# Optimization experiments

Measured on AMD Instinct MI355X. Metric: run time of the kernel, lower is better.

Reference implementation:

```python
import jax, jax.numpy as jnp
import numpy as np

TEMPERATURE = 8.0  # sqrt(head_dim=64)
NEG_INF = -1000000000.0


def setup_inputs() -> dict:
    key = jax.random.key(0)
    kq, kk, kv, km = jax.random.split(key, 4)
    B, H, S, D = 2, 16, 2048, 64
    q = jax.random.normal(kq, (B, H, S, D), dtype=jnp.float32)
    k = jax.random.normal(kk, (B, H, S, D), dtype=jnp.float32)
    v = jax.random.normal(kv, (B, H, S, D), dtype=jnp.float32)
    mask = jax.random.randint(km, (B, 1, S, S), 0, 2, dtype=jnp.int32)
    return {"q": q, "k": k, "v": v, "mask": mask}


def reference(q, k, v, mask):
    # scores: [B,H,S,S] = (q/T) @ k^T
    attn = jnp.einsum('bhqd,bhkd->bhqk', q / TEMPERATURE, k)
    attn = jnp.where(mask == 0, NEG_INF, attn)
    attn = jax.nn.softmax(attn, axis=-1)  # dropout is identity in eval mode
    output = jnp.einsum('bhqk,bhkd->bhqd', attn, v)
    return (output, attn)
```

## Files before the change

kernel.cpp:

```cpp
#include <hip/hip_runtime.h>
#include <hip/hip_bf16.h>


using short4v = __attribute__((ext_vector_type(4))) short;
using short8v = __attribute__((ext_vector_type(8))) short;
using float4v = __attribute__((ext_vector_type(4))) float;

#define S_LEN 2048
#define D_DIM 64
#define QT 64
#define KTILE 64
#define NIT (S_LEN / KTILE)
#define NW (S_LEN / 64)
#define LDK 72
#define ATTN_OFF (2 * 16 * 2048 * 64)
#define TILE_SH (KTILE * D_DIM)

typedef __attribute__((address_space(1))) const unsigned int gu32;
typedef __attribute__((address_space(3))) unsigned int lu32;

__device__ __forceinline__ short f2bf(float x) {
  __hip_bfloat16 h = __float2bfloat16(x);
  return __builtin_bit_cast(short, h);
}
__device__ __forceinline__ float bf2f(short s) {
  return __builtin_bit_cast(float, ((unsigned)(unsigned short)s) << 16);
}

__global__ __launch_bounds__(256) void pack_mask_kernel(
    const int* __restrict__ mask, unsigned long long* __restrict__ pm, int nwords) {
  const int lane = threadIdx.x & 63;
  int gw = (blockIdx.x * blockDim.x + threadIdx.x) >> 6;
  const int stride = (gridDim.x * blockDim.x) >> 6;
  for (int w = gw; w < nwords; w += stride) {
    int m = mask[(size_t)w * 64 + lane];
    unsigned long long bits = __ballot(m != 0);
    if (lane == 0) pm[w] = bits;
  }
}

__global__ __launch_bounds__(256) void kprep_kernel(
    const float* __restrict__ k, short* __restrict__ kbs) {
  int g = blockIdx.x * 256 + threadIdx.x;
  int kr = g >> 3;
  int slot = g & 7;
  const float* src = k + (size_t)kr * D_DIM + ((slot ^ (kr & 7)) << 3);
  float4v a = *(const float4v*)src;
  float4v b = *(const float4v*)(src + 4);
  short8v t;
  t[0] = f2bf(a[0]); t[1] = f2bf(a[1]); t[2] = f2bf(a[2]); t[3] = f2bf(a[3]);
  t[4] = f2bf(b[0]); t[5] = f2bf(b[1]); t[6] = f2bf(b[2]); t[7] = f2bf(b[3]);
  *(short8v*)(kbs + (size_t)g * 8) = t;
}

__global__ __launch_bounds__(256) void vprep_kernel(
    const float* __restrict__ v, short* __restrict__ vts) {
  __shared__ short lds_t[64 * 72];
  const int tid = threadIdx.x;
  const int bh = blockIdx.x >> 5;
  const int kt = blockIdx.x & 31;
  const float* vp = v + ((size_t)bh * S_LEN + kt * KTILE) * D_DIM;
#pragma unroll
  for (int i = 0; i < 4; ++i) {
    int idx = tid + i * 256;
    int s = idx >> 4;
    int d0 = (idx & 15) * 4;
    float4v x = *(const float4v*)(vp + (size_t)s * D_DIM + d0);
#pragma unroll
    for (int j = 0; j < 4; ++j) lds_t[(d0 + j) * 72 + s] = f2bf(x[j]);
  }
  __syncthreads();
  short* dst = vts + (size_t)blockIdx.x * TILE_SH;
#pragma unroll
  for (int i = 0; i < 2; ++i) {
    int g = tid + i * 256;
    int d = g >> 3;
    int slot = g & 7;
    int lsrc = slot ^ (d & 7);
    short8v t = *(const short8v*)(lds_t + d * 72 + lsrc * 8);
    *(short8v*)(dst + g * 8) = t;
  }
}

__device__ __forceinline__ void stage_wave(const short* __restrict__ g, short* l,
                                           int wave, int lane) {
  const short* s0 = g + wave * 1024 + lane * 8;
  short* d0 = l + wave * 1024;
  __builtin_amdgcn_global_load_lds((gu32*)s0, (lu32*)d0, 16, 0, 0);
  __builtin_amdgcn_global_load_lds((gu32*)(s0 + 512), (lu32*)(d0 + 512), 16, 0, 0);
}

__global__ __launch_bounds__(256, 3) void sdpa_fused(
    const float* __restrict__ q, const short* __restrict__ kbs,
    const short* __restrict__ vts, const unsigned long long* __restrict__ pm,
    float* __restrict__ out) {
  __shared__ __align__(16) short lds_k[2][TILE_SH];
  __shared__ __align__(16) short lds_vt[2][TILE_SH];
  __shared__ short lds_p[QT * LDK];

  const int tid  = threadIdx.x;
  const int wave = tid >> 6;
  const int lane = tid & 63;
  const int quad = lane >> 4;
  const int l16  = lane & 15;

  const int blk = (blockIdx.x & 7) * 128 + (blockIdx.x >> 3);
  const int qt  = blk & (NIT - 1);
  const int bh  = blk >> 5;
  const int b   = bh >> 4;

  const float* qp = q + (size_t)bh * S_LEN * D_DIM;
  const short* kb_g = kbs + (size_t)bh * S_LEN * D_DIM;
  const short* vt_g = vts + (size_t)bh * (NIT * TILE_SH);
  float* outO = out + (size_t)bh * S_LEN * D_DIM;
  float* outA = out + (size_t)ATTN_OFF + (size_t)bh * S_LEN * S_LEN;

  const int qbase = qt * QT;
  const int qrowC = qbase + wave * 16 + quad * 4;

  const float QSCALE = 0.18033688011112042f;
  short8v qa[2];
  {
    const int qrow = qbase + wave * 16 + l16;
    const float* src = qp + (size_t)qrow * D_DIM + quad * 8;
#pragma unroll
    for (int c = 0; c < 2; ++c) {
      float4v x0 = *(const float4v*)(src + c * 32);
      float4v x1 = *(const float4v*)(src + c * 32 + 4);
      short8v t;
      t[0] = f2bf(x0[0] * QSCALE); t[1] = f2bf(x0[1] * QSCALE);
      t[2] = f2bf(x0[2] * QSCALE); t[3] = f2bf(x0[3] * QSCALE);
      t[4] = f2bf(x1[0] * QSCALE); t[5] = f2bf(x1[1] * QSCALE);
      t[6] = f2bf(x1[2] * QSCALE); t[7] = f2bf(x1[3] * QSCALE);
      qa[c] = t;
    }
  }

  const unsigned long long* pmrow = pm + ((size_t)b * S_LEN + qrowC) * NW;

  float lsum[4] = {0.f, 0.f, 0.f, 0.f};
  unsigned long long mrow_c[4], mrow_n[4];
#pragma unroll
  for (int r = 0; r < 4; ++r) mrow_c[r] = pmrow[(size_t)r * NW];
  stage_wave(kb_g, lds_k[0], wave, lane);
  __syncthreads();

#pragma unroll 1
  for (int kt = 0; kt < NIT; ++kt) {
    if (kt + 1 < NIT) {
#pragma unroll
      for (int r = 0; r < 4; ++r) mrow_n[r] = pmrow[(size_t)r * NW + kt + 1];
      stage_wave(kb_g + (kt + 1) * TILE_SH, lds_k[(kt + 1) & 1], wave, lane);
    }
    const short* kbuf = lds_k[kt & 1];
#pragma unroll
    for (int t = 0; t < 4; ++t) {
      float4v acc = {0.f, 0.f, 0.f, 0.f};
      const int row = t * 16 + l16;
      const int sw = (row & 7) << 3;
#pragma unroll
      for (int c = 0; c < 2; ++c) {
        short8v bf = *(const short8v*)(kbuf + row * 64 + (((c * 32) + quad * 8) ^ sw));
        acc = __builtin_amdgcn_mfma_f32_16x16x32_bf16(qa[c], bf, acc, 0, 0, 0);
      }
#pragma unroll
      for (int r = 0; r < 4; ++r) {
        bool mv = ((mrow_c[r] >> (t * 16 + l16)) & 1ull) != 0;
        float p = mv ? exp2f(acc[r]) : 0.f;
        lsum[r] += p;
      }
    }
#pragma unroll
    for (int r = 0; r < 4; ++r) mrow_c[r] = mrow_n[r];
    __syncthreads();
  }

  float invl[4];
#pragma unroll
  for (int r = 0; r < 4; ++r) {
    float s = lsum[r];
    s += __shfl_xor(s, 1);
    s += __shfl_xor(s, 2);
    s += __shfl_xor(s, 4);
    s += __shfl_xor(s, 8);
    invl[r] = 1.0f / s;
  }

  float4v oacc[4];
#pragma unroll
  for (int dt = 0; dt < 4; ++dt) oacc[dt] = (float4v){0.f, 0.f, 0.f, 0.f};

#pragma unroll
  for (int r = 0; r < 4; ++r) mrow_c[r] = pmrow[(size_t)r * NW];
  stage_wave(kb_g, lds_k[0], wave, lane);
  stage_wave(vt_g, lds_vt[0], wave, lane);
  __syncthreads();

#pragma unroll 1
  for (int kt = 0; kt < NIT; ++kt) {
    if (kt + 1 < NIT) {
#pragma unroll
      for (int r = 0; r < 4; ++r) mrow_n[r] = pmrow[(size_t)r * NW + kt + 1];
      stage_wave(kb_g + (kt + 1) * TILE_SH, lds_k[(kt + 1) & 1], wave, lane);
      stage_wave(vt_g + (kt + 1) * TILE_SH, lds_vt[(kt + 1) & 1], wave, lane);
    }
    const short* kbuf = lds_k[kt & 1];
    const short* vbuf = lds_vt[kt & 1];

#pragma unroll
    for (int t = 0; t < 4; ++t) {
      float4v acc = {0.f, 0.f, 0.f, 0.f};
      const int row = t * 16 + l16;
      const int sw = (row & 7) << 3;
#pragma unroll
      for (int c = 0; c < 2; ++c) {
        short8v bf = *(const short8v*)(kbuf + row * 64 + (((c * 32) + quad * 8) ^ sw));
        acc = __builtin_amdgcn_mfma_f32_16x16x32_bf16(qa[c], bf, acc, 0, 0, 0);
      }
      short* prow = lds_p + (wave * 16 + quad * 4) * LDK + t * 16 + l16;
#pragma unroll
      for (int r = 0; r < 4; ++r) {
        bool mv = ((mrow_c[r] >> (t * 16 + l16)) & 1ull) != 0;
        float p = mv ? exp2f(acc[r]) * invl[r] : 0.f;
        prow[r * LDK] = f2bf(p);
      }
    }

    {
      const int row16 = lane >> 2;
      const int cg = (lane & 3) * 16;
      const short* src = lds_p + (wave * 16 + row16) * LDK + cg;
      short8v p0 = *(const short8v*)src;
      short8v p1 = *(const short8v*)(src + 8);
      float* arow = outA + (size_t)(qbase + wave * 16 + row16) * S_LEN + kt * KTILE + cg;
      float4v f0 = {bf2f(p0[0]), bf2f(p0[1]), bf2f(p0[2]), bf2f(p0[3])};
      float4v f1 = {bf2f(p0[4]), bf2f(p0[5]), bf2f(p0[6]), bf2f(p0[7])};
      float4v f2 = {bf2f(p1[0]), bf2f(p1[1]), bf2f(p1[2]), bf2f(p1[3])};
      float4v f3 = {bf2f(p1[4]), bf2f(p1[5]), bf2f(p1[6]), bf2f(p1[7])};
      *(float4v*)(arow)      = f0;
      *(float4v*)(arow + 4)  = f1;
      *(float4v*)(arow + 8)  = f2;
      *(float4v*)(arow + 12) = f3;
    }

#pragma unroll
    for (int c = 0; c < 2; ++c) {
      short8v pa = *(const short8v*)(lds_p + (wave * 16 + l16) * LDK + c * 32 + quad * 8);
#pragma unroll
      for (int dt = 0; dt < 4; ++dt) {
        const int row = dt * 16 + l16;
        const int sw = (row & 7) << 3;
        short8v vb = *(const short8v*)(vbuf + row * 64 + (((c * 32) + quad * 8) ^ sw));
        oacc[dt] = __builtin_amdgcn_mfma_f32_16x16x32_bf16(pa, vb, oacc[dt], 0, 0, 0);
      }
    }
#pragma unroll
    for (int r = 0; r < 4; ++r) mrow_c[r] = mrow_n[r];
    __syncthreads();
  }

  {
    float* orow = outO + (size_t)qrowC * D_DIM + l16;
#pragma unroll
    for (int dt = 0; dt < 4; ++dt) {
#pragma unroll
      for (int r = 0; r < 4; ++r) {
        orow[(size_t)r * D_DIM + dt * 16] = oacc[dt][r];
      }
    }
  }
}

template <bool PACKED>
__global__ __launch_bounds__(256, 4) void sdpa_kernel(
    const float* __restrict__ q, const float* __restrict__ k,
    const float* __restrict__ v, const int* __restrict__ mask,
    const unsigned long long* __restrict__ pm, float* __restrict__ out) {
  __shared__ short lds_k[KTILE * LDK];
  __shared__ short lds_vt[D_DIM * LDK];
  __shared__ short lds_p[QT * LDK];

  const int tid  = threadIdx.x;
  const int wave = tid >> 6;
  const int lane = tid & 63;
  const int quad = lane >> 4;
  const int l16  = lane & 15;

  const int blk = blockIdx.x;
  const int qt  = blk & (NIT - 1);
  const int bh  = blk >> 5;
  const int b   = bh >> 4;

  const float* qp = q + (size_t)bh * S_LEN * D_DIM;
  const float* kp = k + (size_t)bh * S_LEN * D_DIM;
  const float* vp = v + (size_t)bh * S_LEN * D_DIM;
  const int*   mp = mask + (size_t)b * S_LEN * S_LEN;
  float* outO = out + (size_t)bh * S_LEN * D_DIM;
  float* outA = out + (size_t)ATTN_OFF + (size_t)bh * S_LEN * S_LEN;

  const int qbase = qt * QT;
  const int qrowC = qbase + wave * 16 + quad * 4;

  const float QSCALE = 0.18033688011112042f;
  short8v qa[2];
  {
    const int qrow = qbase + wave * 16 + l16;
    const float* src = qp + (size_t)qrow * D_DIM + quad * 8;
#pragma unroll
    for (int c = 0; c < 2; ++c) {
      float4v x0 = *(const float4v*)(src + c * 32);
      float4v x1 = *(const float4v*)(src + c * 32 + 4);
      short8v t;
      t[0] = f2bf(x0[0] * QSCALE); t[1] = f2bf(x0[1] * QSCALE);
      t[2] = f2bf(x0[2] * QSCALE); t[3] = f2bf(x0[3] * QSCALE);
      t[4] = f2bf(x1[0] * QSCALE); t[5] = f2bf(x1[1] * QSCALE);
      t[6] = f2bf(x1[2] * QSCALE); t[7] = f2bf(x1[3] * QSCALE);
      qa[c] = t;
    }
  }

  float lsum[4] = {0.f, 0.f, 0.f, 0.f};

#pragma unroll 1
  for (int kt = 0; kt < NIT; ++kt) {
#pragma unroll
    for (int i = 0; i < 4; ++i) {
      int f = tid + i * 256;
      int row = f >> 4;
      int col = (f & 15) * 4;
      float4v x = *(const float4v*)(kp + (size_t)(kt * KTILE + row) * D_DIM + col);
      short4v y;
      y[0] = f2bf(x[0]); y[1] = f2bf(x[1]); y[2] = f2bf(x[2]); y[3] = f2bf(x[3]);
      *(short4v*)(lds_k + row * LDK + col) = y;
    }
    __syncthreads();

    unsigned long long mrow[4];
    if (PACKED) {
#pragma unroll
      for (int r = 0; r < 4; ++r)
        mrow[r] = pm[((size_t)b * S_LEN + qrowC + r) * NW + kt];
    }
#pragma unroll
    for (int t = 0; t < 4; ++t) {
      float4v acc = {0.f, 0.f, 0.f, 0.f};
#pragma unroll
      for (int c = 0; c < 2; ++c) {
        short8v bf = *(const short8v*)(lds_k + (t * 16 + l16) * LDK + c * 32 + quad * 8);
        acc = __builtin_amdgcn_mfma_f32_16x16x32_bf16(qa[c], bf, acc, 0, 0, 0);
      }
      const int kcol = kt * KTILE + t * 16 + l16;
#pragma unroll
      for (int r = 0; r < 4; ++r) {
        bool mv = PACKED ? (((mrow[r] >> (t * 16 + l16)) & 1ull) != 0)
                         : (mp[(size_t)(qrowC + r) * S_LEN + kcol] != 0);
        float p = mv ? exp2f(acc[r]) : 0.f;
        lsum[r] += p;
      }
    }
    __syncthreads();
  }

  float invl[4];
#pragma unroll
  for (int r = 0; r < 4; ++r) {
    float s = lsum[r];
    s += __shfl_xor(s, 1);
    s += __shfl_xor(s, 2);
    s += __shfl_xor(s, 4);
    s += __shfl_xor(s, 8);
    invl[r] = 1.0f / s;
  }

  float4v oacc[4];
#pragma unroll
  for (int dt = 0; dt < 4; ++dt) oacc[dt] = (float4v){0.f, 0.f, 0.f, 0.f};

#pragma unroll 1
  for (int kt = 0; kt < NIT; ++kt) {
#pragma unroll
    for (int i = 0; i < 4; ++i) {
      int f = tid + i * 256;
      int row = f >> 4;
      int col = (f & 15) * 4;
      float4v x = *(const float4v*)(kp + (size_t)(kt * KTILE + row) * D_DIM + col);
      short4v y;
      y[0] = f2bf(x[0]); y[1] = f2bf(x[1]); y[2] = f2bf(x[2]); y[3] = f2bf(x[3]);
      *(short4v*)(lds_k + row * LDK + col) = y;
    }
    {
      const int d = tid & 63;
      const int krg = (tid >> 6) * 4;
#pragma unroll
      for (int i = 0; i < 4; ++i) {
        int kr0 = i * 16 + krg;
        short4v y;
#pragma unroll
        for (int j = 0; j < 4; ++j) {
          float x = vp[(size_t)(kt * KTILE + kr0 + j) * D_DIM + d];
          y[j] = f2bf(x);
        }
        *(short4v*)(lds_vt + d * LDK + kr0) = y;
      }
    }
    __syncthreads();

    unsigned long long mrow[4];
    if (PACKED) {
#pragma unroll
      for (int r = 0; r < 4; ++r)
        mrow[r] = pm[((size_t)b * S_LEN + qrowC + r) * NW + kt];
    }
#pragma unroll
    for (int t = 0; t < 4; ++t) {
      float4v acc = {0.f, 0.f, 0.f, 0.f};
#pragma unroll
      for (int c = 0; c < 2; ++c) {
        short8v bf = *(const short8v*)(lds_k + (t * 16 + l16) * LDK + c * 32 + quad * 8);
        acc = __builtin_amdgcn_mfma_f32_16x16x32_bf16(qa[c], bf, acc, 0, 0, 0);
      }
      const int kcol = kt * KTILE + t * 16 + l16;
      short* prow = lds_p + (wave * 16 + quad * 4) * LDK + t * 16 + l16;
#pragma unroll
      for (int r = 0; r < 4; ++r) {
        bool mv = PACKED ? (((mrow[r] >> (t * 16 + l16)) & 1ull) != 0)
                         : (mp[(size_t)(qrowC + r) * S_LEN + kcol] != 0);
        float p = mv ? exp2f(acc[r]) * invl[r] : 0.f;
        prow[r * LDK] = f2bf(p);
      }
    }

    {
      const int row16 = lane >> 2;
      const int cg = (lane & 3) * 16;
      const short* src = lds_p + (wave * 16 + row16) * LDK + cg;
      short8v p0 = *(const short8v*)src;
      short8v p1 = *(const short8v*)(src + 8);
      float* arow = outA + (size_t)(qbase + wave * 16 + row16) * S_LEN + kt * KTILE + cg;
      float4v f0 = {bf2f(p0[0]), bf2f(p0[1]), bf2f(p0[2]), bf2f(p0[3])};
      float4v f1 = {bf2f(p0[4]), bf2f(p0[5]), bf2f(p0[6]), bf2f(p0[7])};
      float4v f2 = {bf2f(p1[0]), bf2f(p1[1]), bf2f(p1[2]), bf2f(p1[3])};
      float4v f3 = {bf2f(p1[4]), bf2f(p1[5]), bf2f(p1[6]), bf2f(p1[7])};
      *(float4v*)(arow)      = f0;
      *(float4v*)(arow + 4)  = f1;
      *(float4v*)(arow + 8)  = f2;
      *(float4v*)(arow + 12) = f3;
    }

#pragma unroll
    for (int c = 0; c < 2; ++c) {
      short8v pa = *(const short8v*)(lds_p + (wave * 16 + l16) * LDK + c * 32 + quad * 8);
#pragma unroll
      for (int dt = 0; dt < 4; ++dt) {
        short8v vb = *(const short8v*)(lds_vt + (dt * 16 + l16) * LDK + c * 32 + quad * 8);
        oacc[dt] = __builtin_amdgcn_mfma_f32_16x16x32_bf16(pa, vb, oacc[dt], 0, 0, 0);
      }
    }
    __syncthreads();
  }

  {
    float* orow = outO + (size_t)qrowC * D_DIM + l16;
#pragma unroll
    for (int dt = 0; dt < 4; ++dt) {
#pragma unroll
      for (int r = 0; r < 4; ++r) {
        orow[(size_t)r * D_DIM + dt * 16] = oacc[dt][r];
      }
    }
  }
}

extern "C" void kernel_launch(void* const* d_in, const int* in_sizes, int n_in,
                              void* d_out, int out_size, void* d_ws, size_t ws_size,
                              hipStream_t stream) {
  const float* q = (const float*)d_in[0];
  const float* k = (const float*)d_in[1];
  const float* v = (const float*)d_in[2];
  const int* mask = (const int*)d_in[3];
  float* out = (float*)d_out;

  const int BH = 2 * 16;
  dim3 grid(BH * (S_LEN / QT));
  dim3 block(256);

  const int nwords = 2 * S_LEN * NW;
  const size_t pm_bytes = (size_t)nwords * 8;
  const size_t kbs_bytes = (size_t)BH * S_LEN * D_DIM * 2;
  const size_t kbs_off = pm_bytes;
  const size_t vts_off = kbs_off + kbs_bytes;
  const size_t need = vts_off + kbs_bytes;

  if (ws_size >= need) {
    unsigned long long* pm = (unsigned long long*)d_ws;
    short* kbs = (short*)((char*)d_ws + kbs_off);
    short* vts = (short*)((char*)d_ws + vts_off);
    pack_mask_kernel<<<256, 256, 0, stream>>>(mask, pm, nwords);
    kprep_kernel<<<2048, 256, 0, stream>>>(k, kbs);
    vprep_kernel<<<1024, 256, 0, stream>>>(v, vts);
    sdpa_fused<<<grid, block, 0, stream>>>(q, kbs, vts, pm, out);
  } else if (ws_size >= pm_bytes) {
    unsigned long long* pm = (unsigned long long*)d_ws;
    pack_mask_kernel<<<256, 256, 0, stream>>>(mask, pm, nwords);
    sdpa_kernel<true><<<grid, block, 0, stream>>>(q, k, v, mask, pm, out);
  } else {
    sdpa_kernel<false><<<grid, block, 0, stream>>>(q, k, v, mask, nullptr, out);
  }
}
```

Before: 845.5 us.

## Merge prep kernels into one launch and defer nontemporal attention stores

Combines the mask packing, K conversion and V transpose kernels into a single launch that dispatches on block index, removing two kernel launches and their gaps. In the fused SDPA kernel, the fp32 attention-probability stores for each tile are moved to the start of the next iteration so the writes overlap with the next tile's loads and MFMA work. The attention and output writes also become nontemporal stores to avoid polluting the cache. The deferred stores keep extra registers live across iterations, which may affect occupancy.

```diff
diff --git a/kernel.cpp b/kernel.cpp
--- a/kernel.cpp
+++ b/kernel.cpp
@@ -27,6 +27,61 @@
   return __builtin_bit_cast(float, ((unsigned)(unsigned short)s) << 16);
 }
 
+__global__ __launch_bounds__(256) void prep_kernel(
+    const float* __restrict__ k, const float* __restrict__ v,
+    const int* __restrict__ mask, short* __restrict__ kbs,
+    short* __restrict__ vts, unsigned long long* __restrict__ pm, int nwords) {
+  __shared__ short lds_t[64 * 72];
+  const int tid = threadIdx.x;
+  const int bid = blockIdx.x;
+  if (bid < 2048) {
+    int g = bid * 256 + tid;
+    int kr = g >> 3;
+    int slot = g & 7;
+    const float* src = k + (size_t)kr * D_DIM + ((slot ^ (kr & 7)) << 3);
+    float4v a = *(const float4v*)src;
+    float4v b = *(const float4v*)(src + 4);
+    short8v t;
+    t[0] = f2bf(a[0]); t[1] = f2bf(a[1]); t[2] = f2bf(a[2]); t[3] = f2bf(a[3]);
+    t[4] = f2bf(b[0]); t[5] = f2bf(b[1]); t[6] = f2bf(b[2]); t[7] = f2bf(b[3]);
+    *(short8v*)(kbs + (size_t)g * 8) = t;
+  } else if (bid < 3072) {
+    const int vb = bid - 2048;
+    const int bh = vb >> 5;
+    const int kt = vb & 31;
+    const float* vp = v + ((size_t)bh * S_LEN + kt * KTILE) * D_DIM;
+#pragma unroll
+    for (int i = 0; i < 4; ++i) {
+      int idx = tid + i * 256;
+      int s = idx >> 4;
+      int d0 = (idx & 15) * 4;
+      float4v x = *(const float4v*)(vp + (size_t)s * D_DIM + d0);
+#pragma unroll
+      for (int j = 0; j < 4; ++j) lds_t[(d0 + j) * 72 + s] = f2bf(x[j]);
+    }
+    __syncthreads();
+    short* dst = vts + (size_t)vb * TILE_SH;
+#pragma unroll
+    for (int i = 0; i < 2; ++i) {
+      int g = tid + i * 256;
+      int d = g >> 3;
+      int slot = g & 7;
+      int lsrc = slot ^ (d & 7);
+      short8v t = *(const short8v*)(lds_t + d * 72 + lsrc * 8);
+      *(short8v*)(dst + g * 8) = t;
+    }
+  } else {
+    const int lane = tid & 63;
+    int gw = ((bid - 3072) * 256 + tid) >> 6;
+    const int stride = (256 * 256) >> 6;
+    for (int w = gw; w < nwords; w += stride) {
+      int m = mask[(size_t)w * 64 + lane];
+      unsigned long long bits = __ballot(m != 0);
+      if (lane == 0) pm[w] = bits;
+    }
+  }
+}
+
 __global__ __launch_bounds__(256) void pack_mask_kernel(
     const int* __restrict__ mask, unsigned long long* __restrict__ pm, int nwords) {
   const int lane = threadIdx.x & 63;
@@ -39,49 +94,6 @@
   }
 }
 
-__global__ __launch_bounds__(256) void kprep_kernel(
-    const float* __restrict__ k, short* __restrict__ kbs) {
-  int g = blockIdx.x * 256 + threadIdx.x;
-  int kr = g >> 3;
-  int slot = g & 7;
-  const float* src = k + (size_t)kr * D_DIM + ((slot ^ (kr & 7)) << 3);
-  float4v a = *(const float4v*)src;
-  float4v b = *(const float4v*)(src + 4);
-  short8v t;
-  t[0] = f2bf(a[0]); t[1] = f2bf(a[1]); t[2] = f2bf(a[2]); t[3] = f2bf(a[3]);
-  t[4] = f2bf(b[0]); t[5] = f2bf(b[1]); t[6] = f2bf(b[2]); t[7] = f2bf(b[3]);
-  *(short8v*)(kbs + (size_t)g * 8) = t;
-}
-
-__global__ __launch_bounds__(256) void vprep_kernel(
-    const float* __restrict__ v, short* __restrict__ vts) {
-  __shared__ short lds_t[64 * 72];
-  const int tid = threadIdx.x;
-  const int bh = blockIdx.x >> 5;
-  const int kt = blockIdx.x & 31;
-  const float* vp = v + ((size_t)bh * S_LEN + kt * KTILE) * D_DIM;
-#pragma unroll
-  for (int i = 0; i < 4; ++i) {
-    int idx = tid + i * 256;
-    int s = idx >> 4;
-    int d0 = (idx & 15) * 4;
-    float4v x = *(const float4v*)(vp + (size_t)s * D_DIM + d0);
-#pragma unroll
-    for (int j = 0; j < 4; ++j) lds_t[(d0 + j) * 72 + s] = f2bf(x[j]);
-  }
-  __syncthreads();
-  short* dst = vts + (size_t)blockIdx.x * TILE_SH;
-#pragma unroll
-  for (int i = 0; i < 2; ++i) {
-    int g = tid + i * 256;
-    int d = g >> 3;
-    int slot = g & 7;
-    int lsrc = slot ^ (d & 7);
-    short8v t = *(const short8v*)(lds_t + d * 72 + lsrc * 8);
-    *(short8v*)(dst + g * 8) = t;
-  }
-}
-
 __device__ __forceinline__ void stage_wave(const short* __restrict__ g, short* l,
                                            int wave, int lane) {
   const short* s0 = g + wave * 1024 + lane * 8;
@@ -139,7 +151,8 @@
   const unsigned long long* pmrow = pm + ((size_t)b * S_LEN + qrowC) * NW;
 
   float lsum[4] = {0.f, 0.f, 0.f, 0.f};
-  unsigned long long mrow_c[4], mrow_n[4];
+  unsigned long long mrow_c[4];
+  unsigned long long mrow_n[4] = {0ull, 0ull, 0ull, 0ull};
 #pragma unroll
   for (int r = 0; r < 4; ++r) mrow_c[r] = pmrow[(size_t)r * NW];
   stage_wave(kb_g, lds_k[0], wave, lane);
@@ -196,8 +209,24 @@
   stage_wave(vt_g, lds_vt[0], wave, lane);
   __syncthreads();
 
+  const int row16 = lane >> 2;
+  const int cg = (lane & 3) * 16;
+  float* arow_base = outA + (size_t)(qbase + wave * 16 + row16) * S_LEN + cg;
+  short8v pp0, pp1;
+
 #pragma unroll 1
   for (int kt = 0; kt < NIT; ++kt) {
+    if (kt > 0) {
+      float* arow = arow_base + (kt - 1) * KTILE;
+      float4v f0 = {bf2f(pp0[0]), bf2f(pp0[1]), bf2f(pp0[2]), bf2f(pp0[3])};
+      float4v f1 = {bf2f(pp0[4]), bf2f(pp0[5]), bf2f(pp0[6]), bf2f(pp0[7])};
+      float4v f2 = {bf2f(pp1[0]), bf2f(pp1[1]), bf2f(pp1[2]), bf2f(pp1[3])};
+      float4v f3 = {bf2f(pp1[4]), bf2f(pp1[5]), bf2f(pp1[6]), bf2f(pp1[7])};
+      __builtin_nontemporal_store(f0, (float4v*)(arow));
+      __builtin_nontemporal_store(f1, (float4v*)(arow + 4));
+      __builtin_nontemporal_store(f2, (float4v*)(arow + 8));
+      __builtin_nontemporal_store(f3, (float4v*)(arow + 12));
+    }
     if (kt + 1 < NIT) {
 #pragma unroll
       for (int r = 0; r < 4; ++r) mrow_n[r] = pmrow[(size_t)r * NW + kt + 1];
@@ -221,6 +250,211 @@
 #pragma unroll
       for (int r = 0; r < 4; ++r) {
         bool mv = ((mrow_c[r] >> (t * 16 + l16)) & 1ull) != 0;
+        float p = mv ? exp2f(acc[r]) * invl[r] : 0.f;
+        prow[r * LDK] = f2bf(p);
+      }
+    }
+
+    {
+      const short* src = lds_p + (wave * 16 + row16) * LDK + cg;
+      pp0 = *(const short8v*)src;
+      pp1 = *(const short8v*)(src + 8);
+    }
+
+#pragma unroll
+    for (int c = 0; c < 2; ++c) {
+      short8v pa = *(const short8v*)(lds_p + (wave * 16 + l16) * LDK + c * 32 + quad * 8);
+#pragma unroll
+      for (int dt = 0; dt < 4; ++dt) {
+        const int row = dt * 16 + l16;
+        const int sw = (row & 7) << 3;
+        short8v vb = *(const short8v*)(vbuf + row * 64 + (((c * 32) + quad * 8) ^ sw));
+        oacc[dt] = __builtin_amdgcn_mfma_f32_16x16x32_bf16(pa, vb, oacc[dt], 0, 0, 0);
+      }
+    }
+#pragma unroll
+    for (int r = 0; r < 4; ++r) mrow_c[r] = mrow_n[r];
+    __syncthreads();
+  }
+
+  {
+    float* arow = arow_base + (NIT - 1) * KTILE;
+    float4v f0 = {bf2f(pp0[0]), bf2f(pp0[1]), bf2f(pp0[2]), bf2f(pp0[3])};
+    float4v f1 = {bf2f(pp0[4]), bf2f(pp0[5]), bf2f(pp0[6]), bf2f(pp0[7])};
+    float4v f2 = {bf2f(pp1[0]), bf2f(pp1[1]), bf2f(pp1[2]), bf2f(pp1[3])};
+    float4v f3 = {bf2f(pp1[4]), bf2f(pp1[5]), bf2f(pp1[6]), bf2f(pp1[7])};
+    __builtin_nontemporal_store(f0, (float4v*)(arow));
+    __builtin_nontemporal_store(f1, (float4v*)(arow + 4));
+    __builtin_nontemporal_store(f2, (float4v*)(arow + 8));
+    __builtin_nontemporal_store(f3, (float4v*)(arow + 12));
+  }
+
+  {
+    float* orow = outO + (size_t)qrowC * D_DIM + l16;
+#pragma unroll
+    for (int dt = 0; dt < 4; ++dt) {
+#pragma unroll
+      for (int r = 0; r < 4; ++r) {
+        __builtin_nontemporal_store(oacc[dt][r], orow + (size_t)r * D_DIM + dt * 16);
+      }
+    }
+  }
+}
+
+template <bool PACKED>
+__global__ __launch_bounds__(256, 4) void sdpa_kernel(
+    const float* __restrict__ q, const float* __restrict__ k,
+    const float* __restrict__ v, const int* __restrict__ mask,
+    const unsigned long long* __restrict__ pm, float* __restrict__ out) {
+  __shared__ short lds_k[KTILE * LDK];
+  __shared__ short lds_vt[D_DIM * LDK];
+  __shared__ short lds_p[QT * LDK];
+
+  const int tid  = threadIdx.x;
+  const int wave = tid >> 6;
+  const int lane = tid & 63;
+  const int quad = lane >> 4;
+  const int l16  = lane & 15;
+
+  const int blk = blockIdx.x;
+  const int qt  = blk & (NIT - 1);
+  const int bh  = blk >> 5;
+  const int b   = bh >> 4;
+
+  const float* qp = q + (size_t)bh * S_LEN * D_DIM;
+  const float* kp = k + (size_t)bh * S_LEN * D_DIM;
+  const float* vp = v + (size_t)bh * S_LEN * D_DIM;
+  const int*   mp = mask + (size_t)b * S_LEN * S_LEN;
+  float* outO = out + (size_t)bh * S_LEN * D_DIM;
+  float* outA = out + (size_t)ATTN_OFF + (size_t)bh * S_LEN * S_LEN;
+
+  const int qbase = qt * QT;
+  const int qrowC = qbase + wave * 16 + quad * 4;
+
+  const float QSCALE = 0.18033688011112042f;
+  short8v qa[2];
+  {
+    const int qrow = qbase + wave * 16 + l16;
+    const float* src = qp + (size_t)qrow * D_DIM + quad * 8;
+#pragma unroll
+    for (int c = 0; c < 2; ++c) {
+      float4v x0 = *(const float4v*)(src + c * 32);
+      float4v x1 = *(const float4v*)(src + c * 32 + 4);
+      short8v t;
+      t[0] = f2bf(x0[0] * QSCALE); t[1] = f2bf(x0[1] * QSCALE);
+      t[2] = f2bf(x0[2] * QSCALE); t[3] = f2bf(x0[3] * QSCALE);
+      t[4] = f2bf(x1[0] * QSCALE); t[5] = f2bf(x1[1] * QSCALE);
+      t[6] = f2bf(x1[2] * QSCALE); t[7] = f2bf(x1[3] * QSCALE);
+      qa[c] = t;
+    }
+  }
+
+  float lsum[4] = {0.f, 0.f, 0.f, 0.f};
+
+#pragma unroll 1
+  for (int kt = 0; kt < NIT; ++kt) {
+#pragma unroll
+    for (int i = 0; i < 4; ++i) {
+      int f = tid + i * 256;
+      int row = f >> 4;
+      int col = (f & 15) * 4;
+      float4v x = *(const float4v*)(kp + (size_t)(kt * KTILE + row) * D_DIM + col);
+      short4v y;
+      y[0] = f2bf(x[0]); y[1] = f2bf(x[1]); y[2] = f2bf(x[2]); y[3] = f2bf(x[3]);
+      *(short4v*)(lds_k + row * LDK + col) = y;
+    }
+    __syncthreads();
+
+    unsigned long long mrow[4];
+    if (PACKED) {
+#pragma unroll
+      for (int r = 0; r < 4; ++r)
+        mrow[r] = pm[((size_t)b * S_LEN + qrowC + r) * NW + kt];
+    }
+#pragma unroll
+    for (int t = 0; t < 4; ++t) {
+      float4v acc = {0.f, 0.f, 0.f, 0.f};
+#pragma unroll
+      for (int c = 0; c < 2; ++c) {
+        short8v bf = *(const short8v*)(lds_k + (t * 16 + l16) * LDK + c * 32 + quad * 8);
+        acc = __builtin_amdgcn_mfma_f32_16x16x32_bf16(qa[c], bf, acc, 0, 0, 0);
+      }
+      const int kcol = kt * KTILE + t * 16 + l16;
+#pragma unroll
+      for (int r = 0; r < 4; ++r) {
+        bool mv = PACKED ? (((mrow[r] >> (t * 16 + l16)) & 1ull) != 0)
+                         : (mp[(size_t)(qrowC + r) * S_LEN + kcol] != 0);
+        float p = mv ? exp2f(acc[r]) : 0.f;
+        lsum[r] += p;
+      }
+    }
+    __syncthreads();
+  }
+
+  float invl[4];
+#pragma unroll
+  for (int r = 0; r < 4; ++r) {
+    float s = lsum[r];
+    s += __shfl_xor(s, 1);
+    s += __shfl_xor(s, 2);
+    s += __shfl_xor(s, 4);
+    s += __shfl_xor(s, 8);
+    invl[r] = 1.0f / s;
+  }
+
+  float4v oacc[4];
+#pragma unroll
+  for (int dt = 0; dt < 4; ++dt) oacc[dt] = (float4v){0.f, 0.f, 0.f, 0.f};
+
+#pragma unroll 1
+  for (int kt = 0; kt < NIT; ++kt) {
+#pragma unroll
+    for (int i = 0; i < 4; ++i) {
+      int f = tid + i * 256;
+      int row = f >> 4;
+      int col = (f & 15) * 4;
+      float4v x = *(const float4v*)(kp + (size_t)(kt * KTILE + row) * D_DIM + col);
+      short4v y;
+      y[0] = f2bf(x[0]); y[1] = f2bf(x[1]); y[2] = f2bf(x[2]); y[3] = f2bf(x[3]);
+      *(short4v*)(lds_k + row * LDK + col) = y;
+    }
+    {
+      const int d = tid & 63;
+      const int krg = (tid >> 6) * 4;
+#pragma unroll
+      for (int i = 0; i < 4; ++i) {
+        int kr0 = i * 16 + krg;
+        short4v y;
+#pragma unroll
+        for (int j = 0; j < 4; ++j) {
+          float x = vp[(size_t)(kt * KTILE + kr0 + j) * D_DIM + d];
+          y[j] = f2bf(x);
+        }
+        *(short4v*)(lds_vt + d * LDK + kr0) = y;
+      }
+    }
+    __syncthreads();
+
+    unsigned long long mrow[4];
+    if (PACKED) {
+#pragma unroll
+      for (int r = 0; r < 4; ++r)
+        mrow[r] = pm[((size_t)b * S_LEN + qrowC + r) * NW + kt];
+    }
+#pragma unroll
+    for (int t = 0; t < 4; ++t) {
+      float4v acc = {0.f, 0.f, 0.f, 0.f};
+#pragma unroll
+      for (int c = 0; c < 2; ++c) {
+        short8v bf = *(const short8v*)(lds_k + (t * 16 + l16) * LDK + c * 32 + quad * 8);
+        acc = __builtin_amdgcn_mfma_f32_16x16x32_bf16(qa[c], bf, acc, 0, 0, 0);
+      }
+      const int kcol = kt * KTILE + t * 16 + l16;
+      short* prow = lds_p + (wave * 16 + quad * 4) * LDK + t * 16 + l16;
+#pragma unroll
+      for (int r = 0; r < 4; ++r) {
+        bool mv = PACKED ? (((mrow[r] >> (t * 16 + l16)) & 1ull) != 0)
+                         : (mp[(size_t)(qrowC + r) * S_LEN + kcol] != 0);
         float p = mv ? exp2f(acc[r]) * invl[r] : 0.f;
         prow[r * LDK] = f2bf(p);
       }
@@ -248,210 +482,6 @@
       short8v pa = *(const short8v*)(lds_p + (wave * 16 + l16) * LDK + c * 32 + quad * 8);
 #pragma unroll
       for (int dt = 0; dt < 4; ++dt) {
-        const int row = dt * 16 + l16;
-        const int sw = (row & 7) << 3;
-        short8v vb = *(const short8v*)(vbuf + row * 64 + (((c * 32) + quad * 8) ^ sw));
-        oacc[dt] = __builtin_amdgcn_mfma_f32_16x16x32_bf16(pa, vb, oacc[dt], 0, 0, 0);
-      }
-    }
-#pragma unroll
-    for (int r = 0; r < 4; ++r) mrow_c[r] = mrow_n[r];
-    __syncthreads();
-  }
-
-  {
-    float* orow = outO + (size_t)qrowC * D_DIM + l16;
-#pragma unroll
-    for (int dt = 0; dt < 4; ++dt) {
-#pragma unroll
-      for (int r = 0; r < 4; ++r) {
-        orow[(size_t)r * D_DIM + dt * 16] = oacc[dt][r];
-      }
-    }
-  }
-}
-
-template <bool PACKED>
-__global__ __launch_bounds__(256, 4) void sdpa_kernel(
-    const float* __restrict__ q, const float* __restrict__ k,
-    const float* __restrict__ v, const int* __restrict__ mask,
-    const unsigned long long* __restrict__ pm, float* __restrict__ out) {
-  __shared__ short lds_k[KTILE * LDK];
-  __shared__ short lds_vt[D_DIM * LDK];
-  __shared__ short lds_p[QT * LDK];
-
-  const int tid  = threadIdx.x;
-  const int wave = tid >> 6;
-  const int lane = tid & 63;
-  const int quad = lane >> 4;
-  const int l16  = lane & 15;
-
-  const int blk = blockIdx.x;
-  const int qt  = blk & (NIT - 1);
-  const int bh  = blk >> 5;
-  const int b   = bh >> 4;
-
-  const float* qp = q + (size_t)bh * S_LEN * D_DIM;
-  const float* kp = k + (size_t)bh * S_LEN * D_DIM;
-  const float* vp = v + (size_t)bh * S_LEN * D_DIM;
-  const int*   mp = mask + (size_t)b * S_LEN * S_LEN;
-  float* outO = out + (size_t)bh * S_LEN * D_DIM;
-  float* outA = out + (size_t)ATTN_OFF + (size_t)bh * S_LEN * S_LEN;
-
-  const int qbase = qt * QT;
-  const int qrowC = qbase + wave * 16 + quad * 4;
-
-  const float QSCALE = 0.18033688011112042f;
-  short8v qa[2];
-  {
-    const int qrow = qbase + wave * 16 + l16;
-    const float* src = qp + (size_t)qrow * D_DIM + quad * 8;
-#pragma unroll
-    for (int c = 0; c < 2; ++c) {
-      float4v x0 = *(const float4v*)(src + c * 32);
-      float4v x1 = *(const float4v*)(src + c * 32 + 4);
-      short8v t;
-      t[0] = f2bf(x0[0] * QSCALE); t[1] = f2bf(x0[1] * QSCALE);
-      t[2] = f2bf(x0[2] * QSCALE); t[3] = f2bf(x0[3] * QSCALE);
-      t[4] = f2bf(x1[0] * QSCALE); t[5] = f2bf(x1[1] * QSCALE);
-      t[6] = f2bf(x1[2] * QSCALE); t[7] = f2bf(x1[3] * QSCALE);
-      qa[c] = t;
-    }
-  }
-
-  float lsum[4] = {0.f, 0.f, 0.f, 0.f};
-
-#pragma unroll 1
-  for (int kt = 0; kt < NIT; ++kt) {
-#pragma unroll
-    for (int i = 0; i < 4; ++i) {
-      int f = tid + i * 256;
-      int row = f >> 4;
-      int col = (f & 15) * 4;
-      float4v x = *(const float4v*)(kp + (size_t)(kt * KTILE + row) * D_DIM + col);
-      short4v y;
-      y[0] = f2bf(x[0]); y[1] = f2bf(x[1]); y[2] = f2bf(x[2]); y[3] = f2bf(x[3]);
-      *(short4v*)(lds_k + row * LDK + col) = y;
-    }
-    __syncthreads();
-
-    unsigned long long mrow[4];
-    if (PACKED) {
-#pragma unroll
-      for (int r = 0; r < 4; ++r)
-        mrow[r] = pm[((size_t)b * S_LEN + qrowC + r) * NW + kt];
-    }
-#pragma unroll
-    for (int t = 0; t < 4; ++t) {
-      float4v acc = {0.f, 0.f, 0.f, 0.f};
-#pragma unroll
-      for (int c = 0; c < 2; ++c) {
-        short8v bf = *(const short8v*)(lds_k + (t * 16 + l16) * LDK + c * 32 + quad * 8);
-        acc = __builtin_amdgcn_mfma_f32_16x16x32_bf16(qa[c], bf, acc, 0, 0, 0);
-      }
-      const int kcol = kt * KTILE + t * 16 + l16;
-#pragma unroll
-      for (int r = 0; r < 4; ++r) {
-        bool mv = PACKED ? (((mrow[r] >> (t * 16 + l16)) & 1ull) != 0)
-                         : (mp[(size_t)(qrowC + r) * S_LEN + kcol] != 0);
-        float p = mv ? exp2f(acc[r]) : 0.f;
-        lsum[r] += p;
-      }
-    }
-    __syncthreads();
-  }
-
-  float invl[4];
-#pragma unroll
-  for (int r = 0; r < 4; ++r) {
-    float s = lsum[r];
-    s += __shfl_xor(s, 1);
-    s += __shfl_xor(s, 2);
-    s += __shfl_xor(s, 4);
-    s += __shfl_xor(s, 8);
-    invl[r] = 1.0f / s;
-  }
-
-  float4v oacc[4];
-#pragma unroll
-  for (int dt = 0; dt < 4; ++dt) oacc[dt] = (float4v){0.f, 0.f, 0.f, 0.f};
-
-#pragma unroll 1
-  for (int kt = 0; kt < NIT; ++kt) {
-#pragma unroll
-    for (int i = 0; i < 4; ++i) {
-      int f = tid + i * 256;
-      int row = f >> 4;
-      int col = (f & 15) * 4;
-      float4v x = *(const float4v*)(kp + (size_t)(kt * KTILE + row) * D_DIM + col);
-      short4v y;
-      y[0] = f2bf(x[0]); y[1] = f2bf(x[1]); y[2] = f2bf(x[2]); y[3] = f2bf(x[3]);
-      *(short4v*)(lds_k + row * LDK + col) = y;
-    }
-    {
-      const int d = tid & 63;
-      const int krg = (tid >> 6) * 4;
-#pragma unroll
-      for (int i = 0; i < 4; ++i) {
-        int kr0 = i * 16 + krg;
-        short4v y;
-#pragma unroll
-        for (int j = 0; j < 4; ++j) {
-          float x = vp[(size_t)(kt * KTILE + kr0 + j) * D_DIM + d];
-          y[j] = f2bf(x);
-        }
-        *(short4v*)(lds_vt + d * LDK + kr0) = y;
-      }
-    }
-    __syncthreads();
-
-    unsigned long long mrow[4];
-    if (PACKED) {
-#pragma unroll
-      for (int r = 0; r < 4; ++r)
-        mrow[r] = pm[((size_t)b * S_LEN + qrowC + r) * NW + kt];
-    }
-#pragma unroll
-    for (int t = 0; t < 4; ++t) {
-      float4v acc = {0.f, 0.f, 0.f, 0.f};
-#pragma unroll
-      for (int c = 0; c < 2; ++c) {
-        short8v bf = *(const short8v*)(lds_k + (t * 16 + l16) * LDK + c * 32 + quad * 8);
-        acc = __builtin_amdgcn_mfma_f32_16x16x32_bf16(qa[c], bf, acc, 0, 0, 0);
-      }
-      const int kcol = kt * KTILE + t * 16 + l16;
-      short* prow = lds_p + (wave * 16 + quad * 4) * LDK + t * 16 + l16;
-#pragma unroll
-      for (int r = 0; r < 4; ++r) {
-        bool mv = PACKED ? (((mrow[r] >> (t * 16 + l16)) & 1ull) != 0)
-                         : (mp[(size_t)(qrowC + r) * S_LEN + kcol] != 0);
-        float p = mv ? exp2f(acc[r]) * invl[r] : 0.f;
-        prow[r * LDK] = f2bf(p);
-      }
-    }
-
-    {
-      const int row16 = lane >> 2;
-      const int cg = (lane & 3) * 16;
-      const short* src = lds_p + (wave * 16 + row16) * LDK + cg;
-      short8v p0 = *(const short8v*)src;
-      short8v p1 = *(const short8v*)(src + 8);
-      float* arow = outA + (size_t)(qbase + wave * 16 + row16) * S_LEN + kt * KTILE + cg;
-      float4v f0 = {bf2f(p0[0]), bf2f(p0[1]), bf2f(p0[2]), bf2f(p0[3])};
-      float4v f1 = {bf2f(p0[4]), bf2f(p0[5]), bf2f(p0[6]), bf2f(p0[7])};
-      float4v f2 = {bf2f(p1[0]), bf2f(p1[1]), bf2f(p1[2]), bf2f(p1[3])};
-      float4v f3 = {bf2f(p1[4]), bf2f(p1[5]), bf2f(p1[6]), bf2f(p1[7])};
-      *(float4v*)(arow)      = f0;
-      *(float4v*)(arow + 4)  = f1;
-      *(float4v*)(arow + 8)  = f2;
-      *(float4v*)(arow + 12) = f3;
-    }
-
-#pragma unroll
-    for (int c = 0; c < 2; ++c) {
-      short8v pa = *(const short8v*)(lds_p + (wave * 16 + l16) * LDK + c * 32 + quad * 8);
-#pragma unroll
-      for (int dt = 0; dt < 4; ++dt) {
         short8v vb = *(const short8v*)(lds_vt + (dt * 16 + l16) * LDK + c * 32 + quad * 8);
         oacc[dt] = __builtin_amdgcn_mfma_f32_16x16x32_bf16(pa, vb, oacc[dt], 0, 0, 0);
       }
@@ -495,9 +525,7 @@
     unsigned long long* pm = (unsigned long long*)d_ws;
     short* kbs = (short*)((char*)d_ws + kbs_off);
     short* vts = (short*)((char*)d_ws + vts_off);
-    pack_mask_kernel<<<256, 256, 0, stream>>>(mask, pm, nwords);
-    kprep_kernel<<<2048, 256, 0, stream>>>(k, kbs);
-    vprep_kernel<<<1024, 256, 0, stream>>>(v, vts);
+    prep_kernel<<<3328, 256, 0, stream>>>(k, v, mask, kbs, vts, pm, nwords);
     sdpa_fused<<<grid, block, 0, stream>>>(q, kbs, vts, pm, out);
   } else if (ws_size >= pm_bytes) {
     unsigned long long* pm = (unsigned long long*)d_ws;
```

After: 1.104 ms. 30.6% more time.
